# Kernel tuning notes

Hardware: AMD Instinct MI355X
Metric: run time of the kernel (lower is better)

The kernel has to match this reference:

```python
import jax, jax.numpy as jnp
import numpy as np

EPS = 1e-7
MAX_NORM = 1.0 - 1e-3  # projection radius of the unit Poincare ball (c=1)
ALPHA = 0.2            # LeakyReLU negative slope
NEG_INF = -9e15


def _proj(x, max_norm=MAX_NORM):
    # Project points back inside the Poincare ball along the last dim.
    norm = jnp.clip(jnp.linalg.norm(x, axis=-1, keepdims=True), EPS)
    return jnp.where(norm > max_norm, x / norm * max_norm, x)


def _logmap0(x):
    # Log map at the origin of the Poincare ball, c = 1.
    norm = jnp.clip(jnp.linalg.norm(x, axis=-1, keepdims=True), EPS, 1.0 - EPS)
    return jnp.arctanh(norm) * x / norm


def _expmap0(v):
    # Exp map at the origin of the Poincare ball, c = 1.
    norm = jnp.clip(jnp.linalg.norm(v, axis=-1, keepdims=True), EPS)
    return jnp.tanh(norm) * v / norm


def setup_inputs() -> dict:
    key = jax.random.key(0)
    k1, k2, k3 = jax.random.split(key, 3)
    N, D = 12288, 128
    # points strictly inside the ball: ||x|| ~ 0.01*sqrt(128) ~ 0.11 < 1
    x = jax.random.normal(k1, (N, D), dtype=jnp.float32) * 0.01
    adj = jax.random.randint(k2, (N, N), 0, 2, dtype=jnp.int32)
    # attention vector a, as in init: N(0, 0.2) then proj(a, 0.9) row-wise
    a = jax.random.normal(k3, (2 * D, 1), dtype=jnp.float32) * 0.2
    a = _proj(a, 0.9)
    return {"x": x, "adj": adj, "a": a}


def reference(x, adj, a):
    D = a.shape[0] // 2
    x_tan = _logmap0(x)                       # [N, D]
    wh1 = x_tan @ a[:D]                       # [N, 1]
    wh2 = x_tan @ a[D:]                       # [N, 1]
    e = jax.nn.leaky_relu(wh1 + wh2.T, ALPHA)  # [N, N] additive scores
    scores = jnp.where(adj > 0, e, NEG_INF)
    attention = jax.nn.softmax(scores, axis=1)  # dropout omitted (eval mode)
    x_tan_prime = attention @ x_tan            # [N, D]
    return _proj(_expmap0(x_tan_prime))
```

## Files before the change

### kernel.cpp

```cpp
#include <hip/hip_runtime.h>
#include <math.h>

#define NN 12288
#define DD 128
#define EPSF 1e-7f
#define MAXNORM (1.0f - 1e-3f)
#define CSPLIT 8
#define CCOLS (NN / CSPLIT)
#define CSTEPS (CCOLS / 128)
#define SLABS (CSTEPS / 2)

typedef __attribute__((ext_vector_type(8))) short short8_t;
typedef __attribute__((ext_vector_type(4))) float float4_t;
typedef unsigned short ushort_t;

__device__ __forceinline__ unsigned short f2bf(float f) {
    unsigned int u = __builtin_bit_cast(unsigned int, f);
    unsigned int r = u + 0x7FFFu + ((u >> 16) & 1u);
    return (unsigned short)(r >> 16);
}

__global__ __launch_bounds__(128) void prep_kernel(
    const float* __restrict__ x, const float* __restrict__ a,
    ushort_t* __restrict__ xtb,
    float* __restrict__ wh1, float* __restrict__ wh2)
{
    const int r = blockIdx.x;
    const int t = threadIdx.x;
    const float xv = x[r * DD + t];
    const float a1 = a[t];
    const float a2 = a[DD + t];
    float s0 = xv * xv, s1 = xv * a1, s2 = xv * a2;
    #pragma unroll
    for (int o = 32; o > 0; o >>= 1) {
        s0 += __shfl_xor(s0, o);
        s1 += __shfl_xor(s1, o);
        s2 += __shfl_xor(s2, o);
    }
    __shared__ float red[6];
    const int w = t >> 6;
    if ((t & 63) == 0) { red[w * 3 + 0] = s0; red[w * 3 + 1] = s1; red[w * 3 + 2] = s2; }
    __syncthreads();
    const float sumsq = red[0] + red[3];
    const float d1    = red[1] + red[4];
    const float d2    = red[2] + red[5];
    const float nraw  = sqrtf(sumsq);
    const float nrm   = fminf(fmaxf(nraw, EPSF), 1.0f - EPSF);
    const float scale = atanhf(nrm) / nrm;
    xtb[(size_t)r * DD + t] = f2bf(xv * scale);
    if (t == 0) {
        wh1[r] = scale * d1;
        wh2[r] = scale * d2;
    }
}

__global__ __launch_bounds__(256) void swizzle_kernel(
    const ushort_t* __restrict__ xtb, ushort_t* __restrict__ xtB)
{
    __shared__ ushort_t raw[32 * 136];
    const int C = blockIdx.x;
    const int t = threadIdx.x;
    #pragma unroll
    for (int p = 0; p < 2; ++p) {
        const int idx = p * 256 + t;
        const int j = idx >> 4, cell = idx & 15;
        const uint4 v = *(const uint4*)(xtb + (size_t)(C * 32 + j) * DD + cell * 8);
        *(uint4*)&raw[j * 136 + cell * 8] = v;
    }
    __syncthreads();
    #pragma unroll
    for (int p = 0; p < 2; ++p) {
        const int oc = p * 256 + t;
        const int dt = oc >> 6;
        const int l6 = oc & 63;
        const int l15 = l6 & 15, q = l6 >> 4;
        short8_t v;
        #pragma unroll
        for (int e = 0; e < 8; ++e)
            v[e] = (short)raw[(q * 8 + e) * 136 + dt * 16 + l15];
        *(short8_t*)(xtB + (size_t)C * 4096 + oc * 8) = v;
    }
}

__global__ __launch_bounds__(256, 2) void attn_kernel(
    const int* __restrict__ adj,
    const ushort_t* __restrict__ xtB,
    const float* __restrict__ wh1, const float* __restrict__ wh2,
    float* __restrict__ pout, float* __restrict__ plsum)
{
    __shared__ __align__(16) ushort_t B_lds[256 * DD];
    __shared__ __align__(16) float wh2_lds[CCOLS];

    const int t = threadIdx.x;
    const int w = t >> 6, lane = t & 63;
    const int l15 = lane & 15, quad = lane >> 4;
    const int cy = blockIdx.y;
    const int jcol0 = cy * CCOLS;
    const int rowbase = blockIdx.x * 64 + w * 16;

    #pragma unroll
    for (int m = 0; m < CCOLS / 256; ++m)
        wh2_lds[m * 256 + t] = wh2[jcol0 + m * 256 + t];
    const float wh1i = wh1[rowbase + l15];

    const int* adj_lane = adj + (size_t)(rowbase + l15) * NN + jcol0 + quad * 8;
    const uint4* Bsrc = (const uint4*)(xtB + (size_t)(jcol0 >> 5) * 4096);

    float4_t acc[8];
    #pragma unroll
    for (int dt = 0; dt < 8; ++dt) acc[dt] = (float4_t)0.0f;
    float lsum = 0.0f;

    int4 R[8];
    unsigned mCur;

    auto adj_load = [&](int st) {
        const int* bp = adj_lane + st * 128;
        #pragma unroll
        for (int kc = 0; kc < 4; ++kc) {
            R[kc * 2 + 0] = *(const int4*)(bp + kc * 32);
            R[kc * 2 + 1] = *(const int4*)(bp + kc * 32 + 4);
        }
    };

    auto compress = [&]() -> unsigned {
        unsigned m = 0;
        #pragma unroll
        for (int kc = 0; kc < 4; ++kc) {
            const int4 a0 = R[kc * 2 + 0], a1 = R[kc * 2 + 1];
            m |= (a0.x > 0 ? 1u : 0u) << (kc * 8 + 0);
            m |= (a0.y > 0 ? 1u : 0u) << (kc * 8 + 1);
            m |= (a0.z > 0 ? 1u : 0u) << (kc * 8 + 2);
            m |= (a0.w > 0 ? 1u : 0u) << (kc * 8 + 3);
            m |= (a1.x > 0 ? 1u : 0u) << (kc * 8 + 4);
            m |= (a1.y > 0 ? 1u : 0u) << (kc * 8 + 5);
            m |= (a1.z > 0 ? 1u : 0u) << (kc * 8 + 6);
            m |= (a1.w > 0 ? 1u : 0u) << (kc * 8 + 7);
        }
        return m;
    };

    auto stage = [&](int sl) {
        const uint4* gp = Bsrc + (size_t)sl * 4096 + (size_t)w * 64 + lane;
        char* lb = (char*)B_lds + (size_t)w * 64 * 16;
        #pragma unroll
        for (int m = 0; m < 16; ++m) {
            __builtin_amdgcn_global_load_lds(
                (const __attribute__((address_space(1))) unsigned int*)(gp + m * 256),
                (__attribute__((address_space(3))) unsigned int*)(lb + (size_t)m * 256 * 16),
                16, 0, 0);
        }
    };

    auto compute = [&](int st, int par, unsigned mask) {
        #pragma unroll
        for (int kc = 0; kc < 4; ++kc) {
            const unsigned wq = (mask >> (kc * 8)) & 0xFFu;
            const int wbase = st * 128 + kc * 32 + quad * 8;
            const float4 Wa = *(const float4*)&wh2_lds[wbase];
            const float4 Wb = *(const float4*)&wh2_lds[wbase + 4];
            const float u0 = wh1i + Wa.x, u1 = wh1i + Wa.y;
            const float u2 = wh1i + Wa.z, u3 = wh1i + Wa.w;
            const float u4 = wh1i + Wb.x, u5 = wh1i + Wb.y;
            const float u6 = wh1i + Wb.z, u7 = wh1i + Wb.w;
            const float p0 = (wq & 1u)   ? __expf(fmaxf(u0, 0.2f * u0)) : 0.0f;
            const float p1 = (wq & 2u)   ? __expf(fmaxf(u1, 0.2f * u1)) : 0.0f;
            const float p2 = (wq & 4u)   ? __expf(fmaxf(u2, 0.2f * u2)) : 0.0f;
            const float p3 = (wq & 8u)   ? __expf(fmaxf(u3, 0.2f * u3)) : 0.0f;
            const float p4 = (wq & 16u)  ? __expf(fmaxf(u4, 0.2f * u4)) : 0.0f;
            const float p5 = (wq & 32u)  ? __expf(fmaxf(u5, 0.2f * u5)) : 0.0f;
            const float p6 = (wq & 64u)  ? __expf(fmaxf(u6, 0.2f * u6)) : 0.0f;
            const float p7 = (wq & 128u) ? __expf(fmaxf(u7, 0.2f * u7)) : 0.0f;
            lsum += ((p0 + p1) + (p2 + p3)) + ((p4 + p5) + (p6 + p7));
            short8_t af;
            af[0] = (short)f2bf(p0); af[1] = (short)f2bf(p1);
            af[2] = (short)f2bf(p2); af[3] = (short)f2bf(p3);
            af[4] = (short)f2bf(p4); af[5] = (short)f2bf(p5);
            af[6] = (short)f2bf(p6); af[7] = (short)f2bf(p7);
            const ushort_t* Bp = B_lds + (par * 4 + kc) * 4096 + lane * 8;
            #pragma unroll
            for (int dt = 0; dt < 8; ++dt) {
                const short8_t Bf = *(const short8_t*)(Bp + dt * 512);
                acc[dt] = __builtin_amdgcn_mfma_f32_16x16x32_bf16(af, Bf, acc[dt], 0, 0, 0);
            }
        }
    };

    adj_load(0);
    mCur = compress();
    adj_load(1);

    #pragma unroll 1
    for (int sl = 0; sl < SLABS; ++sl) {
        const int st0 = sl * 2;
        __syncthreads();
        stage(sl);
        __syncthreads();
        compute(st0 + 0, 0, mCur);
        mCur = compress();
        if (st0 + 2 < CSTEPS) adj_load(st0 + 2);
        compute(st0 + 1, 1, mCur);
        if (st0 + 2 < CSTEPS) {
            mCur = compress();
            if (st0 + 3 < CSTEPS) adj_load(st0 + 3);
        }
    }

    float v = lsum;
    v += __shfl_xor(v, 16);
    v += __shfl_xor(v, 32);
    if (quad == 0) plsum[(size_t)cy * NN + rowbase + l15] = v;
    #pragma unroll
    for (int dt = 0; dt < 8; ++dt)
        #pragma unroll
        for (int reg = 0; reg < 4; ++reg)
            pout[((size_t)cy * NN + rowbase + quad * 4 + reg) * DD + dt * 16 + l15]
                = acc[dt][reg];
}

__global__ __launch_bounds__(128) void reduce_kernel(
    const float* __restrict__ pout, const float* __restrict__ plsum,
    float* __restrict__ out)
{
    const int i = blockIdx.x;
    const int t = threadIdx.x;
    float v = 0.0f;
    #pragma unroll
    for (int s = 0; s < CSPLIT; ++s) v += pout[((size_t)s * NN + i) * DD + t];
    float ls = 0.0f;
    #pragma unroll
    for (int s = 0; s < CSPLIT; ++s) ls += plsum[(size_t)s * NN + i];
    v /= ls;
    float ss = v * v;
    #pragma unroll
    for (int o = 1; o < 64; o <<= 1) ss += __shfl_xor(ss, o);
    __shared__ float r2[2];
    if ((t & 63) == 0) r2[t >> 6] = ss;
    __syncthreads();
    const float total = r2[0] + r2[1];
    const float nraw = sqrtf(total);
    const float nv   = fmaxf(nraw, EPSF);
    const float th   = tanhf(nv);
    const float ysc  = th / nv;
    const float nyr  = ysc * nraw;
    const float ny   = fmaxf(nyr, EPSF);
    const float psc  = (ny > MAXNORM) ? (MAXNORM / ny) : 1.0f;
    const float os   = ysc * psc;
    out[(size_t)i * DD + t] = v * os;
}

extern "C" void kernel_launch(void* const* d_in, const int* in_sizes, int n_in,
                              void* d_out, int out_size, void* d_ws, size_t ws_size,
                              hipStream_t stream) {
    const float* x   = (const float*)d_in[0];
    const int*   adj = (const int*)d_in[1];
    const float* a   = (const float*)d_in[2];
    float* out = (float*)d_out;

    char* ws = (char*)d_ws;
    ushort_t* xtb = (ushort_t*)ws;  ws += (size_t)NN * DD * sizeof(ushort_t);
    ushort_t* xtB = (ushort_t*)ws;  ws += (size_t)NN * DD * sizeof(ushort_t);
    float* wh1 = (float*)ws;        ws += NN * sizeof(float);
    float* wh2 = (float*)ws;        ws += NN * sizeof(float);
    float* plsum = (float*)ws;      ws += (size_t)CSPLIT * NN * sizeof(float);
    float* pout  = (float*)ws;

    prep_kernel<<<NN, 128, 0, stream>>>(x, a, xtb, wh1, wh2);
    swizzle_kernel<<<NN / 32, 256, 0, stream>>>(xtb, xtB);
    attn_kernel<<<dim3(NN / 64, CSPLIT), 256, 0, stream>>>(
        adj, xtB, wh1, wh2, pout, plsum);
    reduce_kernel<<<NN, 128, 0, stream>>>(pout, plsum, out);
}
```

Baseline: 830.6 us.

## Factor leaky-relu exponent into row and column terms, split MFMA into two branches

The per-element exp of the leaky-relu score is replaced by a factorisation: exp(wh1+wh2) = exp(wh1)*exp(wh2) for the positive branch and exp(0.2*wh1)*exp(0.2*wh2) for the negative branch. Column exponentials are precomputed once per block in LDS as bf16, and the attention matrix is split into two masked operands, each multiplied by B with its own MFMA accumulator and scaled by the row factors at the end. Row sums are also computed by MFMA against a ones vector. This removes the per-element transcendental and float-to-bf16 work but doubles the MFMA count and accumulator registers, which may raise register pressure and hurt occupancy. Precision also changes because bf16 rounding now falls on the column factors rather than on the full product.

Measured after the change: 837.2 us. About the same (+0.8%).

```diff
diff --git a/kernel.cpp b/kernel.cpp
--- a/kernel.cpp
+++ b/kernel.cpp
@@ -90,6 +90,8 @@
 {
     __shared__ __align__(16) ushort_t B_lds[256 * DD];
     __shared__ __align__(16) float wh2_lds[CCOLS];
+    __shared__ __align__(16) ushort_t e2_lds[CCOLS];
+    __shared__ __align__(16) ushort_t e25_lds[CCOLS];
 
     const int t = threadIdx.x;
     const int w = t >> 6, lane = t & 63;
@@ -99,17 +101,34 @@
     const int rowbase = blockIdx.x * 64 + w * 16;
 
     #pragma unroll
-    for (int m = 0; m < CCOLS / 256; ++m)
-        wh2_lds[m * 256 + t] = wh2[jcol0 + m * 256 + t];
+    for (int m = 0; m < CCOLS / 256; ++m) {
+        const float v = wh2[jcol0 + m * 256 + t];
+        wh2_lds[m * 256 + t] = v;
+        e2_lds[m * 256 + t]  = f2bf(__expf(v));
+        e25_lds[m * 256 + t] = f2bf(__expf(0.2f * v));
+    }
     const float wh1i = wh1[rowbase + l15];
+    const float T = -wh1i;
+
+    float c1r[4], c15r[4];
+    #pragma unroll
+    for (int reg = 0; reg < 4; ++reg) {
+        const float wr = wh1[rowbase + quad * 4 + reg];
+        c1r[reg]  = __expf(wr);
+        c15r[reg] = __expf(0.2f * wr);
+    }
 
     const int* adj_lane = adj + (size_t)(rowbase + l15) * NN + jcol0 + quad * 8;
     const uint4* Bsrc = (const uint4*)(xtB + (size_t)(jcol0 >> 5) * 4096);
 
-    float4_t acc[8];
-    #pragma unroll
-    for (int dt = 0; dt < 8; ++dt) acc[dt] = (float4_t)0.0f;
-    float lsum = 0.0f;
+    float4_t accP[8], accN[8], sP, sN;
+    #pragma unroll
+    for (int dt = 0; dt < 8; ++dt) { accP[dt] = (float4_t)0.0f; accN[dt] = (float4_t)0.0f; }
+    sP = (float4_t)0.0f; sN = (float4_t)0.0f;
+
+    short8_t onesf;
+    #pragma unroll
+    for (int e = 0; e < 8; ++e) onesf[e] = (short)0x3F80;
 
     int4 R[8];
     unsigned mCur;
@@ -159,30 +178,34 @@
             const int wbase = st * 128 + kc * 32 + quad * 8;
             const float4 Wa = *(const float4*)&wh2_lds[wbase];
             const float4 Wb = *(const float4*)&wh2_lds[wbase + 4];
-            const float u0 = wh1i + Wa.x, u1 = wh1i + Wa.y;
-            const float u2 = wh1i + Wa.z, u3 = wh1i + Wa.w;
-            const float u4 = wh1i + Wb.x, u5 = wh1i + Wb.y;
-            const float u6 = wh1i + Wb.z, u7 = wh1i + Wb.w;
-            const float p0 = (wq & 1u)   ? __expf(fmaxf(u0, 0.2f * u0)) : 0.0f;
-            const float p1 = (wq & 2u)   ? __expf(fmaxf(u1, 0.2f * u1)) : 0.0f;
-            const float p2 = (wq & 4u)   ? __expf(fmaxf(u2, 0.2f * u2)) : 0.0f;
-            const float p3 = (wq & 8u)   ? __expf(fmaxf(u3, 0.2f * u3)) : 0.0f;
-            const float p4 = (wq & 16u)  ? __expf(fmaxf(u4, 0.2f * u4)) : 0.0f;
-            const float p5 = (wq & 32u)  ? __expf(fmaxf(u5, 0.2f * u5)) : 0.0f;
-            const float p6 = (wq & 64u)  ? __expf(fmaxf(u6, 0.2f * u6)) : 0.0f;
-            const float p7 = (wq & 128u) ? __expf(fmaxf(u7, 0.2f * u7)) : 0.0f;
-            lsum += ((p0 + p1) + (p2 + p3)) + ((p4 + p5) + (p6 + p7));
-            short8_t af;
-            af[0] = (short)f2bf(p0); af[1] = (short)f2bf(p1);
-            af[2] = (short)f2bf(p2); af[3] = (short)f2bf(p3);
-            af[4] = (short)f2bf(p4); af[5] = (short)f2bf(p5);
-            af[6] = (short)f2bf(p6); af[7] = (short)f2bf(p7);
+            const short8_t e2v  = *(const short8_t*)&e2_lds[wbase];
+            const short8_t e25v = *(const short8_t*)&e25_lds[wbase];
+            short8_t afp, afn;
+            afp[0] = ((wq &   1u) && (Wa.x > T)) ? e2v[0] : (short)0;
+            afn[0] = ((wq &   1u) && !(Wa.x > T)) ? e25v[0] : (short)0;
+            afp[1] = ((wq &   2u) && (Wa.y > T)) ? e2v[1] : (short)0;
+            afn[1] = ((wq &   2u) && !(Wa.y > T)) ? e25v[1] : (short)0;
+            afp[2] = ((wq &   4u) && (Wa.z > T)) ? e2v[2] : (short)0;
+            afn[2] = ((wq &   4u) && !(Wa.z > T)) ? e25v[2] : (short)0;
+            afp[3] = ((wq &   8u) && (Wa.w > T)) ? e2v[3] : (short)0;
+            afn[3] = ((wq &   8u) && !(Wa.w > T)) ? e25v[3] : (short)0;
+            afp[4] = ((wq &  16u) && (Wb.x > T)) ? e2v[4] : (short)0;
+            afn[4] = ((wq &  16u) && !(Wb.x > T)) ? e25v[4] : (short)0;
+            afp[5] = ((wq &  32u) && (Wb.y > T)) ? e2v[5] : (short)0;
+            afn[5] = ((wq &  32u) && !(Wb.y > T)) ? e25v[5] : (short)0;
+            afp[6] = ((wq &  64u) && (Wb.z > T)) ? e2v[6] : (short)0;
+            afn[6] = ((wq &  64u) && !(Wb.z > T)) ? e25v[6] : (short)0;
+            afp[7] = ((wq & 128u) && (Wb.w > T)) ? e2v[7] : (short)0;
+            afn[7] = ((wq & 128u) && !(Wb.w > T)) ? e25v[7] : (short)0;
             const ushort_t* Bp = B_lds + (par * 4 + kc) * 4096 + lane * 8;
             #pragma unroll
             for (int dt = 0; dt < 8; ++dt) {
                 const short8_t Bf = *(const short8_t*)(Bp + dt * 512);
-                acc[dt] = __builtin_amdgcn_mfma_f32_16x16x32_bf16(af, Bf, acc[dt], 0, 0, 0);
+                accP[dt] = __builtin_amdgcn_mfma_f32_16x16x32_bf16(afp, Bf, accP[dt], 0, 0, 0);
+                accN[dt] = __builtin_amdgcn_mfma_f32_16x16x32_bf16(afn, Bf, accN[dt], 0, 0, 0);
             }
+            sP = __builtin_amdgcn_mfma_f32_16x16x32_bf16(afp, onesf, sP, 0, 0, 0);
+            sN = __builtin_amdgcn_mfma_f32_16x16x32_bf16(afn, onesf, sN, 0, 0, 0);
         }
     };
 
@@ -206,16 +229,18 @@
         }
     }
 
-    float v = lsum;
-    v += __shfl_xor(v, 16);
-    v += __shfl_xor(v, 32);
-    if (quad == 0) plsum[(size_t)cy * NN + rowbase + l15] = v;
+    #pragma unroll
+    for (int reg = 0; reg < 4; ++reg) {
+        const float ls = c1r[reg] * sP[reg] + c15r[reg] * sN[reg];
+        if (l15 == 0)
+            plsum[(size_t)cy * NN + rowbase + quad * 4 + reg] = ls;
+    }
     #pragma unroll
     for (int dt = 0; dt < 8; ++dt)
         #pragma unroll
         for (int reg = 0; reg < 4; ++reg)
             pout[((size_t)cy * NN + rowbase + quad * 4 + reg) * DD + dt * 16 + l15]
-                = acc[dt][reg];
+                = c1r[reg] * accP[dt][reg] + c15r[reg] * accN[dt][reg];
 }
 
 __global__ __launch_bounds__(128) void reduce_kernel(
```
